# Optimization experiments

Measured on AMD Instinct MI355X. Metric: run time of the kernel, lower is better.

Reference implementation:

```python
import jax, jax.numpy as jnp
import numpy as np

N = 50000      # nodes
E = 800000     # edges per meta-path
P = 3          # meta-paths
IN = 128       # in_size
H = 8          # heads
D = 32         # out_size per head
EMB = 128      # embedding_dim


def setup_inputs() -> dict:
    key = jax.random.key(0)
    ks = jax.random.split(key, 7)
    h = jax.random.normal(ks[0], (N, IN), jnp.float32)
    edge_index = jax.random.randint(ks[1], (P, 2, E), 0, N, dtype=jnp.int32)
    fc_w = jax.random.normal(ks[2], (P, IN, H * D), jnp.float32) * 0.05
    attn_l = jax.random.normal(ks[3], (P, H, D), jnp.float32) * 0.1
    attn_r = jax.random.normal(ks[4], (P, H, D), jnp.float32) * 0.1
    sem_w = jax.random.normal(ks[5], (P * H * D, EMB), jnp.float32) * 0.05
    sem_b = jnp.zeros((EMB,), jnp.float32)
    return {"h": h, "edge_index": edge_index, "fc_w": fc_w,
            "attn_l": attn_l, "attn_r": attn_r, "sem_w": sem_w, "sem_b": sem_b}


def _gat(h, W, al, ar, src, dst):
    # DGL GATConv (no bias/residual), eval mode (no dropout)
    feat = (h @ W).reshape(N, H, D)                      # (N,H,D)
    el = jnp.einsum('nhd,hd->nh', feat, al)              # (N,H)
    er = jnp.einsum('nhd,hd->nh', feat, ar)
    e = jax.nn.leaky_relu(el[src] + er[dst], negative_slope=0.2)  # (E,H)
    # edge softmax over incoming edges of each dst node
    m = jax.ops.segment_max(e, dst, num_segments=N)      # (N,H); -inf only for empty segs (never indexed)
    ex = jnp.exp(e - m[dst])
    den = jax.ops.segment_sum(ex, dst, num_segments=N)   # (N,H)
    a = ex / den[dst]                                    # (E,H)
    msg = feat[src] * a[..., None]                       # (E,H,D) gather + weight
    out = jax.ops.segment_sum(msg, dst, num_segments=N)  # (N,H,D) scatter-add
    return jax.nn.elu(out).reshape(N, H * D)             # flatten(1)


def reference(h, edge_index, fc_w, attn_l, attn_r, sem_w, sem_b):
    src = edge_index[:, 0]  # (P,E)
    dst = edge_index[:, 1]
    # run one GATConv per meta-path, vectorized over the meta-path axis
    z = jax.vmap(_gat, in_axes=(None, 0, 0, 0, 0, 0))(h, fc_w, attn_l, attn_r, src, dst)  # (P,N,H*D)
    z = jnp.transpose(z, (1, 0, 2)).reshape(N, P * H * D)  # stack(dim=1) then reshape [N,-1]
    return z @ sem_w + sem_b                                # SemanticAttention.project2
```

## Files before the change

### kernel.cpp

```cpp
#include <hip/hip_runtime.h>
#include <hip/hip_bf16.h>

#define N_NODES 50000
#define N_EDGES 800000
#define NPATH 3
#define NBKT 196
#define NBKT3 (NPATH * NBKT)
#define NCHUNKBLK 256
#define CHUNK 9375
#define A_STR 264

typedef __attribute__((ext_vector_type(8))) short short8;
typedef __attribute__((ext_vector_type(4))) float v4f;
typedef __attribute__((ext_vector_type(2))) float f2;

__device__ __forceinline__ short f2bf(float v, float* back) {
  unsigned u = __float_as_uint(v);
  unsigned r = (u + 0x7FFFu + ((u >> 16) & 1u)) >> 16;
  *back = __uint_as_float(r << 16);
  return (short)r;
}

__device__ __forceinline__ f2 up2(unsigned u) {
  f2 r;
  r.x = __uint_as_float(u << 16);
  r.y = __uint_as_float(u & 0xFFFF0000u);
  return r;
}

__global__ __launch_bounds__(256) void blk_count_kernel(
    const int* __restrict__ ei, int* __restrict__ cntmat) {
  __shared__ int lcnt[NBKT3];
  const int t = threadIdx.x, blk = blockIdx.x;
  for (int j = t; j < NBKT3; j += 256) lcnt[j] = 0;
  __syncthreads();
  const int lo = blk * CHUNK, hi = lo + CHUNK;
  for (int idx = lo + t; idx < hi; idx += 256) {
    int p = idx / N_EDGES, e = idx - p * N_EDGES;
    int d = ei[p * 2 * N_EDGES + N_EDGES + e];
    atomicAdd(&lcnt[p * NBKT + (d >> 8)], 1);
  }
  __syncthreads();
  for (int j = t; j < NBKT3; j += 256) cntmat[blk * NBKT3 + j] = lcnt[j];
}

__global__ __launch_bounds__(256) void col_scan_kernel(
    const int* __restrict__ cntmat, int* __restrict__ pos, int* __restrict__ btot) {
  __shared__ int tmp[256];
  const int b = blockIdx.x, t = threadIdx.x;
  int v = cntmat[t * NBKT3 + b];
  tmp[t] = v;
  __syncthreads();
  for (int ofs = 1; ofs < 256; ofs <<= 1) {
    int x = (t >= ofs) ? tmp[t - ofs] : 0;
    __syncthreads();
    tmp[t] += x;
    __syncthreads();
  }
  pos[b * 256 + t] = tmp[t] - v;
  if (t == 255) btot[b] = tmp[255];
}

__global__ __launch_bounds__(1024) void bucket_scan_kernel(
    const int* __restrict__ btot, int* __restrict__ boff) {
  __shared__ int tmp[1024];
  const int t = threadIdx.x;
  int v = (t < NBKT3) ? btot[t] : 0;
  tmp[t] = v;
  __syncthreads();
  for (int ofs = 1; ofs < 1024; ofs <<= 1) {
    int x = (t >= ofs) ? tmp[t - ofs] : 0;
    __syncthreads();
    tmp[t] += x;
    __syncthreads();
  }
  if (t < NBKT3) boff[t] = tmp[t] - v;
}

__global__ __launch_bounds__(256) void scatter_det_kernel(
    const int* __restrict__ ei, const int* __restrict__ boff,
    const int* __restrict__ pos, int2* __restrict__ ebuf) {
  __shared__ int cursor[NBKT3];
  const int t = threadIdx.x, blk = blockIdx.x;
  for (int j = t; j < NBKT3; j += 256)
    cursor[j] = boff[j] + pos[j * 256 + blk];
  __syncthreads();
  const int lo = blk * CHUNK, hi = lo + CHUNK;
  for (int idx = lo + t; idx < hi; idx += 256) {
    int p = idx / N_EDGES, e = idx - p * N_EDGES;
    int s = ei[p * 2 * N_EDGES + e];
    int d = ei[p * 2 * N_EDGES + N_EDGES + e];
    int ps = atomicAdd(&cursor[p * NBKT + (d >> 8)], 1);
    ebuf[ps] = make_int2(s, d);
  }
}

__global__ __launch_bounds__(256) void bucket_csr_kernel(
    const int2* __restrict__ ebuf, const int* __restrict__ boff,
    const int* __restrict__ btot,
    int* __restrict__ off3, int* __restrict__ deg3, int* __restrict__ csr_src) {
  __shared__ int cnt[256], excl[256], cur[256];
  const int b = blockIdx.x;
  const int t = threadIdx.x;
  const int p = b / NBKT;
  const int node_base = (b - p * NBKT) * 256;
  const int start = boff[b];
  const int ecount = btot[b];

  cnt[t] = 0;
  __syncthreads();
  for (int i = t; i < ecount; i += 256)
    atomicAdd(&cnt[ebuf[start + i].y & 255], 1);
  __syncthreads();

  int v = cnt[t];
  excl[t] = v;
  __syncthreads();
  for (int ofs = 1; ofs < 256; ofs <<= 1) {
    int x = (t >= ofs) ? excl[t - ofs] : 0;
    __syncthreads();
    excl[t] += x;
    __syncthreads();
  }
  int my_excl = excl[t] - v;
  cur[t] = my_excl;
  const int node = node_base + t;
  if (node < N_NODES) {
    off3[p * N_NODES + node] = start + my_excl;
    deg3[p * N_NODES + node] = v;
  }
  __syncthreads();

  for (int i = t; i < ecount; i += 256) {
    int2 e = ebuf[start + i];
    int pos2 = atomicAdd(&cur[e.y & 255], 1);
    csr_src[start + pos2] = e.x;
  }
}

__global__ __launch_bounds__(256) void prep_kernel(
    const float* __restrict__ fc_w, const float* __restrict__ attn_l,
    const float* __restrict__ attn_r, const float* __restrict__ sem_w,
    __hip_bfloat16* __restrict__ Wf_hi, __hip_bfloat16* __restrict__ Wf_lo,
    __hip_bfloat16* __restrict__ Bs_hi, __hip_bfloat16* __restrict__ Bs_lo) {
  const int p = blockIdx.x / 33;
  const int unit = blockIdx.x % 33;
  const int t = threadIdx.x;
  if (unit < 17) {
    const float* W = fc_w + (size_t)p * 128 * 256;
    int idx = unit * 256 + t;
    int lane = idx & 63;
    int tmp = idx >> 6;
    int nt = tmp % 17, kc = tmp / 17;
    int l15 = lane & 15, quad = lane >> 4;
    __hip_bfloat16* oh = Wf_hi + (size_t)p * 34816;
    __hip_bfloat16* ol = Wf_lo + (size_t)p * 34816;
    for (int j = 0; j < 8; j++) {
      int k = kc * 32 + quad * 8 + j;
      float v;
      if (nt < 16) {
        v = W[k * 256 + nt * 16 + l15];
      } else {
        int h8 = l15 & 7;
        const float* av = ((l15 < 8) ? attn_l : attn_r) + (size_t)p * 256 + h8 * 32;
        v = 0.f;
        for (int dd = 0; dd < 32; dd++)
          v = fmaf(W[k * 256 + h8 * 32 + dd], av[dd], v);
      }
      float back, back2;
      short hb = f2bf(v, &back);
      short lb = f2bf(v - back, &back2);
      ((short*)oh)[(tmp * 64 + lane) * 8 + j] = hb;
      ((short*)ol)[(tmp * 64 + lane) * 8 + j] = lb;
    }
  } else {
    const float* Ws = sem_w + (size_t)p * 256 * 128;
    int idx = (unit - 17) * 256 + t;
    int lane = idx & 63;
    int tmp = idx >> 6;
    int nt = tmp & 7, kc = tmp >> 3;
    int l15 = lane & 15, quad = lane >> 4;
    __hip_bfloat16* oh = Bs_hi + (size_t)p * 32768;
    __hip_bfloat16* ol = Bs_lo + (size_t)p * 32768;
    for (int j = 0; j < 8; j++) {
      int k = kc * 32 + quad * 8 + j;
      float v = Ws[k * 128 + nt * 16 + l15];
      float back, back2;
      short hb = f2bf(v, &back);
      short lb = f2bf(v - back, &back2);
      ((short*)oh)[(tmp * 64 + lane) * 8 + j] = hb;
      ((short*)ol)[(tmp * 64 + lane) * 8 + j] = lb;
    }
  }
}

__global__ __launch_bounds__(64) void feat_mfma_kernel(
    const float* __restrict__ h,
    const __hip_bfloat16* __restrict__ Wf_hi_all,
    const __hip_bfloat16* __restrict__ Wf_lo_all,
    __hip_bfloat16* __restrict__ feat3, float* __restrict__ el3,
    float* __restrict__ er3) {
  const int p = blockIdx.y;
  const __hip_bfloat16* Wf_hi = Wf_hi_all + (size_t)p * 34816;
  const __hip_bfloat16* Wf_lo = Wf_lo_all + (size_t)p * 34816;
  __hip_bfloat16* feat = feat3 + (size_t)p * N_NODES * 256;
  float* el = el3 + (size_t)p * N_NODES * 8;
  float* er = er3 + (size_t)p * N_NODES * 8;

  const int lane = threadIdx.x;
  const int l15 = lane & 15, quad = lane >> 4;
  const int m0 = blockIdx.x * 16;
  const int mrow = m0 + l15;

  v4f acc[17];
#pragma unroll
  for (int nt = 0; nt < 17; nt++) acc[nt] = {0.f, 0.f, 0.f, 0.f};

#pragma unroll
  for (int kc = 0; kc < 4; kc++) {
    const float* hrow = h + (size_t)mrow * 128 + kc * 32 + quad * 8;
    float4 fa = *(const float4*)hrow;
    float4 fb = *(const float4*)(hrow + 4);
    float fv[8] = {fa.x, fa.y, fa.z, fa.w, fb.x, fb.y, fb.z, fb.w};
    short8 ahi, alo;
#pragma unroll
    for (int q = 0; q < 8; q++) {
      float back, back2;
      ahi[q] = f2bf(fv[q], &back);
      alo[q] = f2bf(fv[q] - back, &back2);
    }
#pragma unroll
    for (int nt = 0; nt < 17; nt++) {
      const int o = ((kc * 17 + nt) * 64 + lane) * 8;
      short8 bhi = *(const short8*)(Wf_hi + o);
      short8 blo = *(const short8*)(Wf_lo + o);
      acc[nt] = __builtin_amdgcn_mfma_f32_16x16x32_bf16(ahi, bhi, acc[nt], 0, 0, 0);
      acc[nt] = __builtin_amdgcn_mfma_f32_16x16x32_bf16(ahi, blo, acc[nt], 0, 0, 0);
      acc[nt] = __builtin_amdgcn_mfma_f32_16x16x32_bf16(alo, bhi, acc[nt], 0, 0, 0);
    }
  }

#pragma unroll
  for (int nt = 0; nt < 16; nt++)
#pragma unroll
    for (int r = 0; r < 4; r++) {
      int m = m0 + quad * 4 + r;
      feat[(size_t)m * 256 + nt * 16 + l15] = __float2bfloat16(acc[nt][r]);
    }
#pragma unroll
  for (int r = 0; r < 4; r++) {
    int m = m0 + quad * 4 + r;
    float v = acc[16][r];
    if (l15 < 8) el[m * 8 + l15] = v;
    else         er[m * 8 + (l15 - 8)] = v;
  }
}

__global__ __launch_bounds__(512) void agg_sem_kernel(
    const int* __restrict__ csr_src, const int* __restrict__ off3,
    const int* __restrict__ deg3,
    const float* __restrict__ el3, const float* __restrict__ er3,
    const __hip_bfloat16* __restrict__ feat3,
    const __hip_bfloat16* __restrict__ Bs_hi, const __hip_bfloat16* __restrict__ Bs_lo,
    const float* __restrict__ bias, float* __restrict__ out) {
  __shared__ __align__(16) short Ahi[16 * A_STR];
  __shared__ __align__(16) short Alo[16 * A_STR];
  __shared__ int idxbuf[8 * 128];
  const int t = threadIdx.x;
  const int w = t >> 6, lane = t & 63;
  const int half = lane >> 5;
  const int l5 = lane & 31;
  const int hh = l5 >> 2;
  const int node_base = blockIdx.x * 16;
  const int l15 = lane & 15, quad = lane >> 4;
  const int nt = w;

  v4f acc = {0.f, 0.f, 0.f, 0.f};

  for (int p = 0; p < NPATH; p++) {
    const int* offp = off3 + p * N_NODES;
    const int* degp = deg3 + p * N_NODES;
    const float* elh = el3 + (size_t)p * N_NODES * 8 + hh;
    const float* erp = er3 + (size_t)p * N_NODES * 8;
    const ushort* fpl = (const ushort*)(feat3 + (size_t)p * N_NODES * 256) + l5 * 8;

    const int node0 = node_base + 2 * w;
    const int nA_deg = degp[node0];
    const int nB_deg = degp[node0 + 1];
    const int* LA = csr_src + offp[node0];
    const int* LB = csr_src + offp[node0 + 1];
    {
      int pos = 2 * l5 + half;
      int sb = w * 128 + (half << 5) + l5;
      idxbuf[sb]      = (pos < nA_deg) ? LA[pos] : 0;
      idxbuf[sb + 64] = (pos < nB_deg) ? LB[pos] : 0;
    }

#define LD(S, kk) do {                                                    \
      int2 id_ = *(const int2*)&idxbuf[ib2 + (kk)];                       \
      unsigned ia_ = (unsigned)id_.x, ic_ = (unsigned)id_.y;              \
      x##S##a = elh[ia_ * 8u];                                            \
      x##S##b = elh[ic_ * 8u];                                            \
      f##S##a = *(const uint4*)(fpl + ia_ * 256u);                        \
      f##S##b = *(const uint4*)(fpl + ic_ * 256u);                        \
    } while (0)

#define CN(S, kk) do {                                                    \
      float xx0 = x##S##a + erh;                                          \
      xx0 = fmaxf(xx0, 0.2f * xx0);                                       \
      float e0 = ((kk) < nh) ? __expf(xx0) : 0.f;                         \
      float xx1 = x##S##b + erh;                                          \
      xx1 = fmaxf(xx1, 0.2f * xx1);                                       \
      float e1 = ((kk) + 1 < nh) ? __expf(xx1) : 0.f;                     \
      aD += e0; aD += e1;                                                 \
      f2 e20 = {e0, e0}, e21 = {e1, e1};                                  \
      a0 = __builtin_elementwise_fma(e20, up2(f##S##a.x), a0);            \
      a1 = __builtin_elementwise_fma(e20, up2(f##S##a.y), a1);            \
      a2 = __builtin_elementwise_fma(e20, up2(f##S##a.z), a2);            \
      a3 = __builtin_elementwise_fma(e20, up2(f##S##a.w), a3);            \
      a0 = __builtin_elementwise_fma(e21, up2(f##S##b.x), a0);            \
      a1 = __builtin_elementwise_fma(e21, up2(f##S##b.y), a1);            \
      a2 = __builtin_elementwise_fma(e21, up2(f##S##b.z), a2);            \
      a3 = __builtin_elementwise_fma(e21, up2(f##S##b.w), a3);            \
    } while (0)

#pragma unroll
    for (int i = 0; i < 2; i++) {
      const int node = node0 + i;
      const int n = (i == 0) ? nA_deg : nB_deg;
      const int* lst2 = (i == 0) ? LA : LB;
      const float erh = erp[node * 8 + hh];
      const int ncov = n < 64 ? n : 64;
      const int nh = (ncov - half + 1) >> 1;
      const int nmax = (ncov + 1) >> 1;
      const int ib2 = w * 128 + i * 64 + (half << 5);

      f2 a0 = {0.f, 0.f}, a1 = {0.f, 0.f}, a2 = {0.f, 0.f}, a3 = {0.f, 0.f};
      float aD = 0.f;
      uint4 fAa, fAb, fBa, fBb, fCa, fCb;
      float xAa, xAb, xBa, xBb, xCa, xCb;

      if (nmax > 0) LD(A, 0);
      if (nmax > 2) LD(B, 2);
      if (nmax > 4) LD(C, 4);
      for (int k = 0; k < nmax; k += 6) {
        CN(A, k);
        if (k + 6 < nmax) LD(A, k + 6);
        if (k + 2 < nmax) {
          CN(B, k + 2);
          if (k + 8 < nmax) LD(B, k + 8);
          if (k + 4 < nmax) {
            CN(C, k + 4);
            if (k + 10 < nmax) LD(C, k + 10);
          }
        }
      }
      if (n > 64) {
        for (int j = 64; j < n; j += 2) {
          int v = (j + half) < n;
          unsigned su = v ? (unsigned)lst2[j + half] : 0u;
          float x = elh[su * 8u];
          uint4 f = *(const uint4*)(fpl + su * 256u);
          float xx = x + erh;
          xx = fmaxf(xx, 0.2f * xx);
          float e = v ? __expf(xx) : 0.f;
          aD += e;
          f2 e2t = {e, e};
          a0 = __builtin_elementwise_fma(e2t, up2(f.x), a0);
          a1 = __builtin_elementwise_fma(e2t, up2(f.y), a1);
          a2 = __builtin_elementwise_fma(e2t, up2(f.z), a2);
          a3 = __builtin_elementwise_fma(e2t, up2(f.w), a3);
        }
      }

      float aN[8] = {a0.x, a0.y, a1.x, a1.y, a2.x, a2.y, a3.x, a3.y};
#pragma unroll
      for (int k = 0; k < 8; k++) aN[k] += __shfl_xor(aN[k], 32, 64);
      aD += __shfl_xor(aD, 32, 64);

      float inv = (n > 0) ? 1.f / aD : 0.f;
      short8 hi8, lo8;
#pragma unroll
      for (int k = 0; k < 8; k++) {
        float r = aN[k] * inv;
        r = r > 0.f ? r : (__expf(r) - 1.f);
        float back, back2;
        hi8[k] = f2bf(r, &back);
        lo8[k] = f2bf(r - back, &back2);
      }
      const int row = 2 * w + i;
      short* dst = half ? Alo : Ahi;
      short8 vv = half ? lo8 : hi8;
      *(short8*)&dst[row * A_STR + l5 * 8] = vv;
    }
#undef LD
#undef CN
    __syncthreads();

    const __hip_bfloat16* bh = Bs_hi + (size_t)p * 32768;
    const __hip_bfloat16* bl = Bs_lo + (size_t)p * 32768;
#pragma unroll
    for (int kc = 0; kc < 8; kc++) {
      short8 ahi = *(const short8*)&Ahi[l15 * A_STR + kc * 32 + quad * 8];
      short8 alo = *(const short8*)&Alo[l15 * A_STR + kc * 32 + quad * 8];
      const int o = ((kc * 8 + nt) * 64 + lane) * 8;
      short8 bhi = *(const short8*)(bh + o);
      short8 blo = *(const short8*)(bl + o);
      acc = __builtin_amdgcn_mfma_f32_16x16x32_bf16(ahi, bhi, acc, 0, 0, 0);
      acc = __builtin_amdgcn_mfma_f32_16x16x32_bf16(ahi, blo, acc, 0, 0, 0);
      acc = __builtin_amdgcn_mfma_f32_16x16x32_bf16(alo, bhi, acc, 0, 0, 0);
    }
    __syncthreads();
  }

  const float bv = bias[nt * 16 + l15];
#pragma unroll
  for (int r = 0; r < 4; r++) {
    int m = node_base + quad * 4 + r;
    out[(size_t)m * 128 + nt * 16 + l15] = acc[r] + bv;
  }
}

extern "C" void kernel_launch(void* const* d_in, const int* in_sizes, int n_in,
                              void* d_out, int out_size, void* d_ws, size_t ws_size,
                              hipStream_t stream) {
  const float* h      = (const float*)d_in[0];
  const int*   ei     = (const int*)d_in[1];
  const float* fc_w   = (const float*)d_in[2];
  const float* attn_l = (const float*)d_in[3];
  const float* attn_r = (const float*)d_in[4];
  const float* sem_w  = (const float*)d_in[5];
  const float* sem_b  = (const float*)d_in[6];
  float* out = (float*)d_out;

  char* ws = (char*)d_ws;
  __hip_bfloat16* feat3 = (__hip_bfloat16*)ws;
  float* el3     = (float*)(ws + 76800000);
  float* er3     = (float*)(ws + 81600000);
  int*   csr_src = (int*)(ws + 86400000);
  int2*  ebuf    = (int2*)(ws + 96000000);
  int*   deg3    = (int*)(ws + 115200000);
  int*   off3    = (int*)(ws + 115800000);
  int*   cntmat  = (int*)(ws + 116400000);
  int*   posm    = (int*)(ws + 117050000);
  int*   btot    = (int*)(ws + 117700000);
  int*   boff    = (int*)(ws + 117710000);
  __hip_bfloat16* Wf_hi = (__hip_bfloat16*)(ws + 117800000);
  __hip_bfloat16* Wf_lo = (__hip_bfloat16*)(ws + 118050000);
  __hip_bfloat16* Bs_hi = (__hip_bfloat16*)(ws + 118300000);
  __hip_bfloat16* Bs_lo = (__hip_bfloat16*)(ws + 118550000);

  blk_count_kernel<<<NCHUNKBLK, 256, 0, stream>>>(ei, cntmat);
  col_scan_kernel<<<NBKT3, 256, 0, stream>>>(cntmat, posm, btot);
  bucket_scan_kernel<<<1, 1024, 0, stream>>>(btot, boff);
  scatter_det_kernel<<<NCHUNKBLK, 256, 0, stream>>>(ei, boff, posm, ebuf);
  bucket_csr_kernel<<<NBKT3, 256, 0, stream>>>(ebuf, boff, btot, off3, deg3, csr_src);
  prep_kernel<<<NPATH * 33, 256, 0, stream>>>(fc_w, attn_l, attn_r, sem_w,
                                              Wf_hi, Wf_lo, Bs_hi, Bs_lo);

  feat_mfma_kernel<<<dim3(N_NODES / 16, NPATH), 64, 0, stream>>>(
      h, Wf_hi, Wf_lo, feat3, el3, er3);

  agg_sem_kernel<<<N_NODES / 16, 512, 0, stream>>>(
      csr_src, off3, deg3, el3, er3, feat3, Bs_hi, Bs_lo, sem_b, out);
}
```

Measured before the change: 469.5 us.

## Shrink aggregation blocks to 8 nodes and trim load pipeline depth

The fused aggregation and semantic-projection kernel now runs 256-thread blocks over 8 nodes instead of 512 threads over 16. Each wave computes two MFMA output column tiles, and the unused upper 8 rows of the A tile are zero-filled. The gather prefetch depth drops from three staged loads to two, and launch bounds ask for 8 blocks per CU. Together these lower register pressure and raise occupancy, but half of each MFMA's work is now wasted on the zero rows and the B weights are loaded per block twice as often.

After: 634.1 us. +35.1%, slower.

```diff
diff --git a/kernel.cpp b/kernel.cpp
--- a/kernel.cpp
+++ b/kernel.cpp
@@ -256,7 +256,7 @@
   }
 }
 
-__global__ __launch_bounds__(512) void agg_sem_kernel(
+__global__ __launch_bounds__(256, 8) void agg_sem_kernel(
     const int* __restrict__ csr_src, const int* __restrict__ off3,
     const int* __restrict__ deg3,
     const float* __restrict__ el3, const float* __restrict__ er3,
@@ -265,17 +265,22 @@
     const float* __restrict__ bias, float* __restrict__ out) {
   __shared__ __align__(16) short Ahi[16 * A_STR];
   __shared__ __align__(16) short Alo[16 * A_STR];
-  __shared__ int idxbuf[8 * 128];
+  __shared__ int idxbuf[4 * 128];
   const int t = threadIdx.x;
   const int w = t >> 6, lane = t & 63;
   const int half = lane >> 5;
   const int l5 = lane & 31;
   const int hh = l5 >> 2;
-  const int node_base = blockIdx.x * 16;
+  const int node_base = blockIdx.x * 8;
   const int l15 = lane & 15, quad = lane >> 4;
-  const int nt = w;
-
-  v4f acc = {0.f, 0.f, 0.f, 0.f};
+
+  for (int j = t; j < 8 * A_STR; j += 256) {
+    Ahi[8 * A_STR + j] = 0;
+    Alo[8 * A_STR + j] = 0;
+  }
+
+  v4f acc0 = {0.f, 0.f, 0.f, 0.f};
+  v4f acc1 = {0.f, 0.f, 0.f, 0.f};
 
   for (int p = 0; p < NPATH; p++) {
     const int* offp = off3 + p * N_NODES;
@@ -337,22 +342,17 @@
 
       f2 a0 = {0.f, 0.f}, a1 = {0.f, 0.f}, a2 = {0.f, 0.f}, a3 = {0.f, 0.f};
       float aD = 0.f;
-      uint4 fAa, fAb, fBa, fBb, fCa, fCb;
-      float xAa, xAb, xBa, xBb, xCa, xCb;
+      uint4 fAa, fAb, fBa, fBb;
+      float xAa, xAb, xBa, xBb;
 
       if (nmax > 0) LD(A, 0);
       if (nmax > 2) LD(B, 2);
-      if (nmax > 4) LD(C, 4);
-      for (int k = 0; k < nmax; k += 6) {
+      for (int k = 0; k < nmax; k += 4) {
         CN(A, k);
-        if (k + 6 < nmax) LD(A, k + 6);
+        if (k + 4 < nmax) LD(A, k + 4);
         if (k + 2 < nmax) {
           CN(B, k + 2);
-          if (k + 8 < nmax) LD(B, k + 8);
-          if (k + 4 < nmax) {
-            CN(C, k + 4);
-            if (k + 10 < nmax) LD(C, k + 10);
-          }
+          if (k + 6 < nmax) LD(B, k + 6);
         }
       }
       if (n > 64) {
@@ -399,25 +399,37 @@
 
     const __hip_bfloat16* bh = Bs_hi + (size_t)p * 32768;
     const __hip_bfloat16* bl = Bs_lo + (size_t)p * 32768;
+    const int nt0 = 2 * w, nt1 = 2 * w + 1;
 #pragma unroll
     for (int kc = 0; kc < 8; kc++) {
       short8 ahi = *(const short8*)&Ahi[l15 * A_STR + kc * 32 + quad * 8];
       short8 alo = *(const short8*)&Alo[l15 * A_STR + kc * 32 + quad * 8];
-      const int o = ((kc * 8 + nt) * 64 + lane) * 8;
-      short8 bhi = *(const short8*)(bh + o);
-      short8 blo = *(const short8*)(bl + o);
-      acc = __builtin_amdgcn_mfma_f32_16x16x32_bf16(ahi, bhi, acc, 0, 0, 0);
-      acc = __builtin_amdgcn_mfma_f32_16x16x32_bf16(ahi, blo, acc, 0, 0, 0);
-      acc = __builtin_amdgcn_mfma_f32_16x16x32_bf16(alo, bhi, acc, 0, 0, 0);
-    }
-    __syncthreads();
-  }
-
-  const float bv = bias[nt * 16 + l15];
-#pragma unroll
-  for (int r = 0; r < 4; r++) {
-    int m = node_base + quad * 4 + r;
-    out[(size_t)m * 128 + nt * 16 + l15] = acc[r] + bv;
+      const int o0 = ((kc * 8 + nt0) * 64 + lane) * 8;
+      const int o1 = ((kc * 8 + nt1) * 64 + lane) * 8;
+      short8 bhi0 = *(const short8*)(bh + o0);
+      short8 blo0 = *(const short8*)(bl + o0);
+      short8 bhi1 = *(const short8*)(bh + o1);
+      short8 blo1 = *(const short8*)(bl + o1);
+      acc0 = __builtin_amdgcn_mfma_f32_16x16x32_bf16(ahi, bhi0, acc0, 0, 0, 0);
+      acc0 = __builtin_amdgcn_mfma_f32_16x16x32_bf16(ahi, blo0, acc0, 0, 0, 0);
+      acc0 = __builtin_amdgcn_mfma_f32_16x16x32_bf16(alo, bhi0, acc0, 0, 0, 0);
+      acc1 = __builtin_amdgcn_mfma_f32_16x16x32_bf16(ahi, bhi1, acc1, 0, 0, 0);
+      acc1 = __builtin_amdgcn_mfma_f32_16x16x32_bf16(ahi, blo1, acc1, 0, 0, 0);
+      acc1 = __builtin_amdgcn_mfma_f32_16x16x32_bf16(alo, bhi1, acc1, 0, 0, 0);
+    }
+    __syncthreads();
+  }
+
+  if (quad < 2) {
+    const int nt0 = 2 * w, nt1 = 2 * w + 1;
+    const float bv0 = bias[nt0 * 16 + l15];
+    const float bv1 = bias[nt1 * 16 + l15];
+#pragma unroll
+    for (int r = 0; r < 4; r++) {
+      int m = node_base + quad * 4 + r;
+      out[(size_t)m * 128 + nt0 * 16 + l15] = acc0[r] + bv0;
+      out[(size_t)m * 128 + nt1 * 16 + l15] = acc1[r] + bv1;
+    }
   }
 }
 
@@ -461,6 +473,6 @@
   feat_mfma_kernel<<<dim3(N_NODES / 16, NPATH), 64, 0, stream>>>(
       h, Wf_hi, Wf_lo, feat3, el3, er3);
 
-  agg_sem_kernel<<<N_NODES / 16, 512, 0, stream>>>(
+  agg_sem_kernel<<<N_NODES / 8, 256, 0, stream>>>(
       csr_src, off3, deg3, el3, er3, feat3, Bs_hi, Bs_lo, sem_b, out);
 }
```
